# Optimization experiments

Hardware: AMD Instinct MI355X
Metric: run time of the kernel (lower is better)

## Reference

```python
import jax, jax.numpy as jnp
import numpy as np

# Module constants derived from default grid_config
D = 59          # depth bins: (60-1)/1
C_OUT = 64
X, Y, Z = 128, 128, 7
STRIDE = 16
GRID_LB = np.array([-51.2, -51.2, -2.5], dtype=np.float32)
GRID_IV = np.array([0.8, 0.8, 1.0], dtype=np.float32)
D0, DSTEP = 1.0, 1.0

B, N, C_IN, H, W = 4, 6, 256, 16, 44


def _voxel_coords():
    xs, ys, zs = np.meshgrid(np.arange(X), np.arange(Y), np.arange(Z), indexing='ij')
    coords = np.stack([xs, ys, zs], axis=-1).reshape(-1, 3).astype(np.float32)
    coords = coords * GRID_IV + GRID_LB  # [V, 3] ego-frame voxel centers
    return coords


def _camera_rig(rng):
    """Realistic 6-camera rig: yawed cameras looking outward, z_cam = forward."""
    c2e = np.zeros((B, N, 4, 4), dtype=np.float32)
    K = np.zeros((B, N, 3, 3), dtype=np.float32)
    for b in range(B):
        for n in range(N):
            a = 2.0 * np.pi * n / N + 0.02 * rng.standard_normal()
            f = np.array([np.cos(a), np.sin(a), 0.0])           # camera forward (z_cam)
            x_cam = np.array([-np.sin(a), np.cos(a), 0.0])      # camera right
            y_cam = np.array([0.0, 0.0, -1.0])                   # camera down
            R = np.stack([x_cam, y_cam, f], axis=1)              # columns = cam axes in ego
            t = 1.0 * f + np.array([0.0, 0.0, 1.5])
            c2e[b, n, :3, :3] = R
            c2e[b, n, :3, 3] = t
            c2e[b, n, 3, 3] = 1.0
            fl = 400.0 + 5.0 * rng.standard_normal()
            K[b, n] = np.array([[fl, 0.0, 352.0], [0.0, fl, 128.0], [0.0, 0.0, 1.0]])
    return c2e, K


def setup_inputs() -> dict:
    key = jax.random.key(0)
    k1, k2, k3 = jax.random.split(key, 3)
    img_feats = jax.random.normal(k1, (B, N, C_IN, H, W), dtype=jnp.float32)
    c2e, K = _camera_rig(np.random.default_rng(0))
    # depth_net: 1x1 conv in_channels -> D + C_OUT
    w_depth = jax.random.normal(k2, (D + C_OUT, C_IN), dtype=jnp.float32) * (1.0 / np.sqrt(C_IN))
    b_depth = jax.random.normal(k3, (D + C_OUT,), dtype=jnp.float32) * 0.01
    return {
        'img_feats': img_feats,
        'cam2ego': jnp.asarray(c2e),
        'cam_intrinsics': jnp.asarray(K),
        'w_depth': w_depth,
        'b_depth': b_depth,
    }


def reference(img_feats, cam2ego, cam_intrinsics, w_depth, b_depth):
    Bc, Nc, C, Hc, Wc = img_feats.shape
    # 1x1 conv == per-pixel linear
    x = jnp.einsum('bnchw,oc->bnhwo', img_feats, w_depth) + b_depth  # [B,N,H,W,D+C_OUT]
    depth = jax.nn.softmax(x[..., :D], axis=-1)                      # [B,N,H,W,D]
    feat = x[..., D:]                                                # [B,N,H,W,C_OUT]

    vox = jnp.asarray(_voxel_coords())                               # [V,3]
    V = vox.shape[0]
    vox_h = jnp.concatenate([vox, jnp.ones((V, 1), vox.dtype)], axis=1)  # [V,4]

    e2c = jnp.linalg.inv(cam2ego)                                    # [B,N,4,4]
    cam = jnp.einsum('bnij,vj->bnvi', e2c, vox_h)[..., :3]           # [B,N,V,3]
    z = cam[..., 2]
    z_safe = jnp.maximum(z, 0.1)
    norm = cam[..., :2] / z_safe[..., None]
    homo = jnp.concatenate([norm, jnp.ones_like(z[..., None])], axis=-1)  # [B,N,V,3]
    img = jnp.einsum('bnij,bnvj->bnvi', cam_intrinsics, homo)[..., :2]
    fc = img / STRIDE                                                # feature-plane coords

    depth_bin = ((z - D0) / DSTEP).astype(jnp.int32)                 # trunc toward 0, matches .long()
    valid = (
        (fc[..., 0] >= 0) & (fc[..., 0] < Wc)
        & (fc[..., 1] >= 0) & (fc[..., 1] < Hc)
        & (z > 0.5)
        & (depth_bin >= 0) & (depth_bin < D)
    )

    u = jnp.clip(fc[..., 0].astype(jnp.int32), 0, Wc - 1)            # [B,N,V]
    v = jnp.clip(fc[..., 1].astype(jnp.int32), 0, Hc - 1)
    d = jnp.clip(depth_bin, 0, D - 1)
    hw = v * Wc + u

    feat_flat = feat.reshape(Bc, Nc, Hc * Wc, C_OUT)
    sampled_feat = jnp.take_along_axis(feat_flat, hw[..., None], axis=2)   # [B,N,V,C_OUT]
    depth_flat = depth.reshape(Bc, Nc, Hc * Wc * D)
    sampled_depth = jnp.take_along_axis(depth_flat, hw * D + d, axis=2)    # [B,N,V]

    wgt = sampled_depth * valid.astype(sampled_depth.dtype)
    # scatter_add at flat_idx == voxel index (identity) -> masked sum over cameras
    bev = jnp.einsum('bnv,bnvc->bvc', wgt, sampled_feat)             # [B,V,C_OUT]
    bev = bev.reshape(Bc, X, Y, Z, C_OUT).sum(axis=3)                # collapse Z
    bev = bev.transpose(0, 3, 2, 1)                                  # [B,C_OUT,Y,X]
    return bev, depth
```

## Files before the change

### kernel.cpp

```cpp
#include <hip/hip_runtime.h>
#include <math.h>

#define D_BINS 59
#define CO     64
#define CI     256
#define NB     4
#define NC     6
#define H_IMG  16
#define W_IMG  44
#define HW     704
#define NPIX   (NB*NC*HW)
#define XD     128
#define YD     128
#define ZD     7
#define NOUT   123
#define PXB    66
#define ABUF   4224

typedef float v2f __attribute__((ext_vector_type(2)));

__device__ void inv_rigid(const float* __restrict__ M, float* __restrict__ o) {
    double a = M[0], b = M[1], c = M[2], t0 = M[3];
    double d = M[4], e = M[5], f = M[6], t1 = M[7];
    double g = M[8], h = M[9], ii = M[10], t2 = M[11];
    double A00 = e*ii - f*h, A01 = c*h - b*ii, A02 = b*f - c*e;
    double A10 = f*g - d*ii, A11 = a*ii - c*g, A12 = c*d - a*f;
    double A20 = d*h - e*g,  A21 = b*g - a*h,  A22 = a*e - b*d;
    double det = a*A00 + b*A10 + c*A20;
    double inv = 1.0 / det;
    double r00 = A00*inv, r01 = A01*inv, r02 = A02*inv;
    double r10 = A10*inv, r11 = A11*inv, r12 = A12*inv;
    double r20 = A20*inv, r21 = A21*inv, r22 = A22*inv;
    o[0] = (float)r00; o[1] = (float)r01; o[2]  = (float)r02;
    o[3] = (float)(-(r00*t0 + r01*t1 + r02*t2));
    o[4] = (float)r10; o[5] = (float)r11; o[6]  = (float)r12;
    o[7] = (float)(-(r10*t0 + r11*t1 + r12*t2));
    o[8] = (float)r20; o[9] = (float)r21; o[10] = (float)r22;
    o[11] = (float)(-(r20*t0 + r21*t1 + r22*t2));
}

__global__ __launch_bounds__(256) void k_pre(
    const float* __restrict__ wd, const float* __restrict__ c2e,
    float* __restrict__ wt2, float* __restrict__ e2c) {
    const int o = blockIdx.x;
    const int k = threadIdx.x;
    float v = (o < NOUT) ? wd[(size_t)o * CI + k] : 0.f;
    wt2[(size_t)(k >> 1) * 256 + o * 2 + (k & 1)] = v;
    if (blockIdx.x == 0 && k < NB * NC)
        inv_rigid(c2e + k * 16, e2c + k * 12);
}

__global__ __launch_bounds__(640) void k_head(
    const float* __restrict__ img, const float* __restrict__ wt2,
    const float* __restrict__ bd, float* __restrict__ depth_out,
    float* __restrict__ feat_ws) {
    __shared__ float smem[PXB * 132 + PXB];
    float* S = smem + PXB * 132;

    const int tid = threadIdx.x;
    const int wv  = tid >> 6;
    const int ln  = tid & 63;
    const int p0  = blockIdx.x * PXB;
    const bool is_main = (wv < 8);
    const int o0  = __builtin_amdgcn_readfirstlane((is_main ? wv : 0) << 4);
    const int epx = 64 + (wv - 8);

    int a_off[7];
    int g_off[7];
#pragma unroll
    for (int it = 0; it < 7; ++it) {
        int idx = tid + it * 640;
        if (idx < 64 * PXB) {
            int kl = idx / PXB, px = idx - kl * PXB;
            int p = p0 + px;
            int bn = p / HW, hw = p - bn * HW;
            a_off[it] = (kl >> 1) * 132 + px * 2 + (kl & 1);
            g_off[it] = (bn * CI + kl) * HW + hw;
        } else {
            a_off[it] = -1;
            g_off[it] = 0;
        }
    }

    v2f acc[16];
#pragma unroll
    for (int j = 0; j < 16; ++j) acc[j] = (v2f)(0.f);
    v2f acc2a = (v2f)(0.f), acc2b = (v2f)(0.f);

#pragma unroll
    for (int it = 0; it < 7; ++it)
        if (a_off[it] >= 0) smem[a_off[it]] = img[g_off[it]];
    __syncthreads();

    for (int kc = 0; kc < 4; ++kc) {
        const float* A = smem + (kc & 1) * ABUF;
        float* An = smem + ((kc + 1) & 1) * ABUF;

        float r[7];
        if (kc < 3) {
#pragma unroll
            for (int it = 0; it < 7; ++it)
                if (a_off[it] >= 0)
                    r[it] = img[g_off[it] + (kc + 1) * 64 * HW];
        }

        if (is_main) {
#pragma unroll 4
            for (int k2 = 0; k2 < 32; ++k2) {
                v2f a = *(const v2f*)(A + k2 * 132 + ln * 2);
                const v2f* w =
                    (const v2f*)(wt2 + (size_t)(kc * 32 + k2) * 256) + o0;
#pragma unroll
                for (int j = 0; j < 16; ++j)
                    acc[j] = __builtin_elementwise_fma(a, w[j], acc[j]);
            }
        } else {
#pragma unroll 4
            for (int k2 = 0; k2 < 32; ++k2) {
                v2f a = *(const v2f*)(A + k2 * 132 + epx * 2);
                const float* w = wt2 + (size_t)(kc * 32 + k2) * 256;
                v2f w0 = {w[ln * 2], w[ln * 2 + 1]};
                v2f w1 = {w[(ln + 64) * 2], w[(ln + 64) * 2 + 1]};
                acc2a = __builtin_elementwise_fma(a, w0, acc2a);
                acc2b = __builtin_elementwise_fma(a, w1, acc2b);
            }
        }

        if (kc < 3) {
#pragma unroll
            for (int it = 0; it < 7; ++it)
                if (a_off[it] >= 0) An[a_off[it]] = r[it];
        }
        __syncthreads();
    }

    float* X = smem;
    if (is_main) {
#pragma unroll
        for (int j = 0; j < 16; ++j) {
            int o = o0 + j;
            if (o < NOUT) {
                int col = (o < D_BINS) ? o : o + 5;
                X[ln * 132 + col] = (acc[j].x + acc[j].y) + bd[o];
            }
        }
    } else {
        int o = ln;
        X[epx * 132 + ((o < D_BINS) ? o : o + 5)] = (acc2a.x + acc2a.y) + bd[o];
        o = ln + 64;
        if (o < NOUT)
            X[epx * 132 + ((o < D_BINS) ? o : o + 5)] = (acc2b.x + acc2b.y) + bd[o];
    }
    __syncthreads();

#pragma unroll
    for (int it = 0; it < 2; ++it) {
        int g = tid + it * 640;
        if (g < PXB * 16) {
            int p = g >> 4, m = g & 15;
            float4 v = *(const float4*)(X + p * 132 + 64 + m * 4);
            *(float4*)(feat_ws + (size_t)(p0 + p) * CO + m * 4) = v;
        }
    }

    if (tid < PXB) {
        float* row = X + tid * 132;
        float m = row[0];
        for (int o = 1; o < D_BINS; ++o) m = fmaxf(m, row[o]);
        float s = 0.f;
        for (int o = 0; o < D_BINS; ++o) {
            float e = __expf(row[o] - m);
            row[o] = e;
            s += e;
        }
        S[tid] = 1.f / s;
    }
    __syncthreads();

    for (int g = tid; g < PXB * D_BINS; g += 640) {
        int p = g / D_BINS;
        int o = g - p * D_BINS;
        depth_out[(size_t)p0 * D_BINS + g] = X[p * 132 + o] * S[p];
    }
}

__global__ __launch_bounds__(256) void k_splat(
    const float* __restrict__ e2c, const float* __restrict__ Kmat,
    const float* __restrict__ depth_g, const float* __restrict__ feat_ws,
    float* __restrict__ bev) {
    __shared__ int   hw_s[ZD][64];
    __shared__ float wgt_s[ZD][64];

    const int tx = threadIdx.x;
    const int cq = threadIdx.y;
    const int x = blockIdx.x * 64 + tx;
    const int y = blockIdx.y;
    const int b = blockIdx.z;
    const float wx = (float)x * 0.8f + (-51.2f);
    const float wy = (float)y * 0.8f + (-51.2f);

    float acc[16];
#pragma unroll
    for (int m = 0; m < 16; ++m) acc[m] = 0.f;

    for (int n = 0; n < NC; ++n) {
        const int bn = b * NC + n;
        const float* E = e2c + bn * 12;
        const float* Km = Kmat + bn * 9;
        const float k00 = Km[0], k01 = Km[1], k02 = Km[2];
        const float k10 = Km[3], k11 = Km[4], k12 = Km[5];
        const float e02 = E[2], e12 = E[6], e22 = E[10];
        const float bx0 = E[0] * wx + E[1] * wy + E[3];
        const float bx1 = E[4] * wx + E[5] * wy + E[7];
        const float bx2 = E[8] * wx + E[9] * wy + E[11];

#pragma unroll
        for (int zz = 0; zz < 2; ++zz) {
            const int z = cq + zz * 4;
            if (z < ZD) {
                const float wz = -2.5f + (float)z;
                const float cx = bx0 + e02 * wz;
                const float cy = bx1 + e12 * wz;
                const float cz = bx2 + e22 * wz;
                const float zs = fmaxf(cz, 0.1f);
                const float rz = 1.0f / zs;
                const float xn = cx * rz;
                const float yn = cy * rz;
                const float fu = (k00 * xn + k01 * yn + k02) * 0.0625f;
                const float fv = (k10 * xn + k11 * yn + k12) * 0.0625f;
                const int bin = (int)(cz - 1.0f);
                const bool valid = (fu >= 0.f) & (fu < (float)W_IMG) &
                                   (fv >= 0.f) & (fv < (float)H_IMG) &
                                   (cz > 0.5f) & (bin >= 0) & (bin < D_BINS);
                int hw = -1;
                float wgt = 0.f;
                if (valid) {
                    int u = (int)fu;
                    int v = (int)fv;
                    hw = v * W_IMG + u;
                    wgt = depth_g[((size_t)bn * HW + hw) * D_BINS + bin];
                }
                hw_s[z][tx] = hw;
                wgt_s[z][tx] = wgt;
            }
        }
        __syncthreads();

#pragma unroll
        for (int z = 0; z < ZD; ++z) {
            const int hw = hw_s[z][tx];
            if (hw >= 0) {
                const float wgt = wgt_s[z][tx];
                const float4* fp =
                    (const float4*)(feat_ws + ((size_t)bn * HW + hw) * CO + cq * 16);
                float4 f0 = fp[0], f1 = fp[1], f2 = fp[2], f3 = fp[3];
                acc[0]  = fmaf(wgt, f0.x, acc[0]);
                acc[1]  = fmaf(wgt, f0.y, acc[1]);
                acc[2]  = fmaf(wgt, f0.z, acc[2]);
                acc[3]  = fmaf(wgt, f0.w, acc[3]);
                acc[4]  = fmaf(wgt, f1.x, acc[4]);
                acc[5]  = fmaf(wgt, f1.y, acc[5]);
                acc[6]  = fmaf(wgt, f1.z, acc[6]);
                acc[7]  = fmaf(wgt, f1.w, acc[7]);
                acc[8]  = fmaf(wgt, f2.x, acc[8]);
                acc[9]  = fmaf(wgt, f2.y, acc[9]);
                acc[10] = fmaf(wgt, f2.z, acc[10]);
                acc[11] = fmaf(wgt, f2.w, acc[11]);
                acc[12] = fmaf(wgt, f3.x, acc[12]);
                acc[13] = fmaf(wgt, f3.y, acc[13]);
                acc[14] = fmaf(wgt, f3.z, acc[14]);
                acc[15] = fmaf(wgt, f3.w, acc[15]);
            }
        }
        __syncthreads();
    }
    float* ob = bev + (((size_t)b * CO + cq * 16) * YD + y) * XD + x;
#pragma unroll
    for (int m = 0; m < 16; ++m) ob[(size_t)m * YD * XD] = acc[m];
}

extern "C" void kernel_launch(void* const* d_in, const int* in_sizes, int n_in,
                              void* d_out, int out_size, void* d_ws, size_t ws_size,
                              hipStream_t stream) {
    const float* img  = (const float*)d_in[0];
    const float* c2e  = (const float*)d_in[1];
    const float* Kmat = (const float*)d_in[2];
    const float* wd   = (const float*)d_in[3];
    const float* bd   = (const float*)d_in[4];
    float* bev = (float*)d_out;
    float* depth_out = bev + (size_t)NB * CO * YD * XD;
    float* feat_ws = (float*)d_ws;
    float* wt2 = feat_ws + (size_t)NPIX * CO;
    float* e2c = wt2 + 128 * 256;

    k_pre<<<128, 256, 0, stream>>>(wd, c2e, wt2, e2c);
    k_head<<<256, 640, 0, stream>>>(img, wt2, bd, depth_out, feat_ws);
    k_splat<<<dim3(2, YD, NB), dim3(64, 4, 1), 0, stream>>>(e2c, Kmat, depth_out,
                                                            feat_ws, bev);
}
```

Measured before the change: 124.2 us.

## Stage depth-head weight chunks in LDS and single-buffer activation tiles

Each K-chunk of the transposed weight matrix (8192 floats) is now prefetched into registers and staged in shared memory alongside the activation tile. The inner loop reads weights from LDS as float4 instead of issuing scalar/vector global loads for every k step. Activation double-buffering is replaced by a single buffer with an extra barrier per chunk, and shared memory use grows by about 32KB, which may reduce occupancy and serializes the store behind compute.

```diff
diff --git a/kernel.cpp b/kernel.cpp
--- a/kernel.cpp
+++ b/kernel.cpp
@@ -16,6 +16,8 @@
 #define NOUT   123
 #define PXB    66
 #define ABUF   4224
+#define WOFF   ABUF
+#define WCHUNK 8192
 
 typedef float v2f __attribute__((ext_vector_type(2)));
 
@@ -54,8 +56,8 @@
     const float* __restrict__ img, const float* __restrict__ wt2,
     const float* __restrict__ bd, float* __restrict__ depth_out,
     float* __restrict__ feat_ws) {
-    __shared__ float smem[PXB * 132 + PXB];
-    float* S = smem + PXB * 132;
+    __shared__ float smem[ABUF + WCHUNK + PXB];
+    float* S = smem + ABUF + WCHUNK;
 
     const int tid = threadIdx.x;
     const int wv  = tid >> 6;
@@ -87,51 +89,79 @@
     for (int j = 0; j < 16; ++j) acc[j] = (v2f)(0.f);
     v2f acc2a = (v2f)(0.f), acc2b = (v2f)(0.f);
 
+    float  ra[7];
+    float4 rw[4];
+
 #pragma unroll
     for (int it = 0; it < 7; ++it)
-        if (a_off[it] >= 0) smem[a_off[it]] = img[g_off[it]];
+        if (a_off[it] >= 0) ra[it] = img[g_off[it]];
+#pragma unroll
+    for (int it = 0; it < 4; ++it) {
+        int idx = tid + it * 640;
+        if (idx < WCHUNK / 4) rw[it] = ((const float4*)wt2)[idx];
+    }
+#pragma unroll
+    for (int it = 0; it < 7; ++it)
+        if (a_off[it] >= 0) smem[a_off[it]] = ra[it];
+#pragma unroll
+    for (int it = 0; it < 4; ++it) {
+        int idx = tid + it * 640;
+        if (idx < WCHUNK / 4) ((float4*)(smem + WOFF))[idx] = rw[it];
+    }
     __syncthreads();
 
     for (int kc = 0; kc < 4; ++kc) {
-        const float* A = smem + (kc & 1) * ABUF;
-        float* An = smem + ((kc + 1) & 1) * ABUF;
-
-        float r[7];
         if (kc < 3) {
 #pragma unroll
             for (int it = 0; it < 7; ++it)
                 if (a_off[it] >= 0)
-                    r[it] = img[g_off[it] + (kc + 1) * 64 * HW];
+                    ra[it] = img[g_off[it] + (kc + 1) * 64 * HW];
+#pragma unroll
+            for (int it = 0; it < 4; ++it) {
+                int idx = tid + it * 640;
+                if (idx < WCHUNK / 4)
+                    rw[it] = ((const float4*)(wt2 + (size_t)(kc + 1) * WCHUNK))[idx];
+            }
         }
 
         if (is_main) {
 #pragma unroll 4
             for (int k2 = 0; k2 < 32; ++k2) {
-                v2f a = *(const v2f*)(A + k2 * 132 + ln * 2);
-                const v2f* w =
-                    (const v2f*)(wt2 + (size_t)(kc * 32 + k2) * 256) + o0;
-#pragma unroll
-                for (int j = 0; j < 16; ++j)
-                    acc[j] = __builtin_elementwise_fma(a, w[j], acc[j]);
+                v2f a = *(const v2f*)(smem + k2 * 132 + ln * 2);
+                const float* wr = smem + WOFF + k2 * 256 + o0 * 2;
+#pragma unroll
+                for (int jj = 0; jj < 8; ++jj) {
+                    float4 wq = *(const float4*)(wr + jj * 4);
+                    v2f w0 = {wq.x, wq.y};
+                    v2f w1 = {wq.z, wq.w};
+                    acc[jj * 2]     = __builtin_elementwise_fma(a, w0, acc[jj * 2]);
+                    acc[jj * 2 + 1] = __builtin_elementwise_fma(a, w1, acc[jj * 2 + 1]);
+                }
             }
         } else {
 #pragma unroll 4
             for (int k2 = 0; k2 < 32; ++k2) {
-                v2f a = *(const v2f*)(A + k2 * 132 + epx * 2);
-                const float* w = wt2 + (size_t)(kc * 32 + k2) * 256;
-                v2f w0 = {w[ln * 2], w[ln * 2 + 1]};
-                v2f w1 = {w[(ln + 64) * 2], w[(ln + 64) * 2 + 1]};
+                v2f a = *(const v2f*)(smem + k2 * 132 + epx * 2);
+                const float* wr = smem + WOFF + k2 * 256;
+                v2f w0 = *(const v2f*)(wr + ln * 2);
+                v2f w1 = *(const v2f*)(wr + (ln + 64) * 2);
                 acc2a = __builtin_elementwise_fma(a, w0, acc2a);
                 acc2b = __builtin_elementwise_fma(a, w1, acc2b);
             }
         }
+        __syncthreads();
 
         if (kc < 3) {
 #pragma unroll
             for (int it = 0; it < 7; ++it)
-                if (a_off[it] >= 0) An[a_off[it]] = r[it];
-        }
-        __syncthreads();
+                if (a_off[it] >= 0) smem[a_off[it]] = ra[it];
+#pragma unroll
+            for (int it = 0; it < 4; ++it) {
+                int idx = tid + it * 640;
+                if (idx < WCHUNK / 4) ((float4*)(smem + WOFF))[idx] = rw[it];
+            }
+            __syncthreads();
+        }
     }
 
     float* X = smem;
```

After: 141.1 us. 13.6% more time.
